# Performance work log

Measured on AMD Instinct MI355X. Metric: run time of the kernel, lower is better.

## Reference

```python
import jax, jax.numpy as jnp
import numpy as np

B, H, W, C = 4, 64, 64, 64
GROUPS = 32
EPS = 1e-3  # keras GroupNormalization default


def setup_inputs() -> dict:
    key = jax.random.key(0)
    ks = jax.random.split(key, 6)
    s = 1.0 / np.sqrt(C)
    return {
        'x': jax.random.normal(ks[0], (B, H, W, C), dtype=jnp.float32),
        'gamma': jnp.ones((C,), jnp.float32),
        'beta': jnp.zeros((C,), jnp.float32),
        'wq': jax.random.uniform(ks[1], (C, C), jnp.float32, -s, s),
        'bq': jnp.zeros((C,), jnp.float32),
        'wk': jax.random.uniform(ks[2], (C, C), jnp.float32, -s, s),
        'bk': jnp.zeros((C,), jnp.float32),
        'wv': jax.random.uniform(ks[3], (C, C), jnp.float32, -s, s),
        'bv': jnp.zeros((C,), jnp.float32),
        'wo': jnp.zeros((C, C), jnp.float32),  # init_scale=0.0 -> ~zero init
        'bo': jnp.zeros((C,), jnp.float32),
    }


def group_norm(x, gamma, beta):
    b, h, w, c = x.shape
    xg = x.reshape(b, h, w, GROUPS, c // GROUPS)
    mean = jnp.mean(xg, axis=(1, 2, 4), keepdims=True)
    var = jnp.var(xg, axis=(1, 2, 4), keepdims=True)
    xn = ((xg - mean) * jax.lax.rsqrt(var + EPS)).reshape(b, h, w, c)
    return xn * gamma + beta


def reference(x, gamma, beta, wq, bq, wk, bk, wv, bv, wo, bo):
    b, h, w, c = x.shape
    hn = group_norm(x, gamma, beta)
    # 1x1 convs == per-pixel dense layers
    q = jnp.einsum('bhwc,cd->bhwd', hn, wq) + bq
    k = jnp.einsum('bhwc,cd->bhwd', hn, wk) + bk
    v = jnp.einsum('bhwc,cd->bhwd', hn, wv) + bv
    # full spatial attention scores [B,H,W,H,W]
    scores = jnp.einsum('bhwc,bHWc->bhwHW', q, k) * (float(c) ** -0.5)
    attn = jax.nn.softmax(scores.reshape(b, h, w, h * w), axis=-1)
    attn = attn.reshape(b, h, w, h, w)
    o = jnp.einsum('bhwHW,bHWc->bhwc', attn, v)
    o = jnp.einsum('bhwc,cd->bhwd', o, wo) + bo
    return x + o
```

## Files before the change

kernel.cpp:

```cpp
#include <hip/hip_runtime.h>
#include <math.h>

#define BB 4
#define HH 64
#define WW 64
#define CC 64
#define NN (HH*WW)
#define NPIX (BB*NN)
#define EPS 1e-3f
#define QBLK 32
#define KSPLIT 8
#define NQT32 (NPIX/QBLK)
#define NCHK ((NN/KSPLIT)/64)

using bf16x8 = __attribute__((ext_vector_type(8))) short;
using f32x4  = __attribute__((ext_vector_type(4))) float;
using f32x16 = __attribute__((ext_vector_type(16))) float;

__device__ inline unsigned short bf16bits(float f) {
    union { float f; unsigned u; } a; a.f = f;
    unsigned r = a.u + 0x7fffu + ((a.u >> 16) & 1u);
    return (unsigned short)(r >> 16);
}
__device__ inline unsigned packbf(float lo, float hi) {
    return (unsigned)bf16bits(lo) | ((unsigned)bf16bits(hi) << 16);
}
__device__ inline unsigned cvtpk(float lo, float hi) {
    unsigned r;
    asm("v_cvt_pk_bf16_f32 %0, %1, %2" : "=v"(r) : "v"(lo), "v"(hi));
    return r;
}
#define PSWAP(a, b) asm("v_permlane32_swap_b32 %0, %1" : "+v"(a), "+v"(b))

__device__ __forceinline__ float exp2g(float x) { return exp2f(x); }

#define QSCALE 0.18033688011112042f

__global__ __launch_bounds__(256) void gn_wt(const float* __restrict__ x,
                                             float* __restrict__ part,
                                             const float* __restrict__ wq,
                                             const float* __restrict__ wk,
                                             const float* __restrict__ wv,
                                             const float* __restrict__ wo,
                                             short* __restrict__ wfrag) {
    int t = threadIdx.x;
    if (blockIdx.x < 256) {
        int c = t & 63, rr = t >> 6;
        int p0 = blockIdx.x * 64;
        float s = 0.f, s2 = 0.f;
        #pragma unroll
        for (int k = 0; k < 16; ++k) {
            float v = x[(size_t)(p0 + rr + 4 * k) * CC + c];
            s += v; s2 += v * v;
        }
        __shared__ float sA[256], sB[256];
        sA[t] = s; sB[t] = s2;
        __syncthreads();
        if (t < 64) {
            float fs  = sA[t] + sA[64 + t] + sA[128 + t] + sA[192 + t];
            float fs2 = sB[t] + sB[64 + t] + sB[128 + t] + sB[192 + t];
            part[blockIdx.x * 128 + t]      = fs;
            part[blockIdx.x * 128 + 64 + t] = fs2;
        }
    } else {
        const float* mats[3] = {wq, wk, wv};
        int i0 = (blockIdx.x - 256) * 256 + t;
        for (int e = i0; e < 12288; e += 16 * 256) {
            int m = e >> 12;
            int r = e & 4095;
            int dt = r >> 10, h = (r >> 9) & 1, lane = (r >> 3) & 63, j = r & 7;
            int g = lane >> 4, cl = lane & 15;
            float v = mats[m][(h * 32 + g * 8 + j) * 64 + dt * 16 + cl];
            wfrag[e] = (short)bf16bits(v);
        }
        for (int e = i0; e < 4096; e += 16 * 256) {
            int j = e & 7, lane = (e >> 3) & 63, dt = (e >> 9) & 1, s = e >> 10;
            int hi = lane >> 5, l31 = lane & 31;
            float v = wo[(8 * hi + 16 * s + j) * 64 + dt * 32 + l31];
            wfrag[12288 + e] = (short)bf16bits(v);
        }
    }
}

__global__ __launch_bounds__(256) void gn_final(const float* __restrict__ part,
                                                const float* __restrict__ gamma,
                                                const float* __restrict__ beta,
                                                float* __restrict__ scale,
                                                float* __restrict__ shift) {
    int b = blockIdx.x;
    int t = threadIdx.x;
    int c = t & 63, rr = t >> 6;
    float s = 0.f, s2 = 0.f;
    #pragma unroll
    for (int k = 0; k < 16; ++k) {
        int blk = b * 64 + rr + 4 * k;
        s  += part[blk * 128 + c];
        s2 += part[blk * 128 + 64 + c];
    }
    __shared__ float sA[256], sB[256];
    sA[t] = s; sB[t] = s2;
    __syncthreads();
    if (t < 64) {
        sA[t] = sA[t] + sA[64 + t] + sA[128 + t] + sA[192 + t];
        sB[t] = sB[t] + sB[64 + t] + sB[128 + t] + sB[192 + t];
    }
    __syncthreads();
    if (t < 64) {
        int g = t >> 1;
        float sumg  = sA[g * 2] + sA[g * 2 + 1];
        float sum2g = sB[g * 2] + sB[g * 2 + 1];
        const float n = (float)(NN * 2);
        float mean = sumg / n;
        float var  = sum2g / n - mean * mean;
        float r = rsqrtf(var + EPS);
        float a = gamma[t] * r;
        scale[b * CC + t] = a;
        shift[b * CC + t] = beta[t] - mean * a;
    }
}

__global__ __launch_bounds__(256) void qkv_proj(
        const float* __restrict__ x,
        const float* __restrict__ scale,
        const float* __restrict__ shift,
        const short* __restrict__ wfrag,
        const float* __restrict__ bq, const float* __restrict__ bk,
        const float* __restrict__ bv,
        short* __restrict__ qb, short* __restrict__ kb,
        short* __restrict__ vt) {
    __shared__ unsigned short vtile[64 * 72];
    int t = threadIdx.x;
    int lane = t & 63, wid = t >> 6;
    int g = lane >> 4, cl = lane & 15;
    int pixblk = blockIdx.x * 64;
    int pix0 = pixblk + wid * 16;
    int b = pixblk >> 12;

    const float* xp = x + (size_t)(pix0 + cl) * CC + g * 8;
    float4 x00 = *(const float4*)(xp);
    float4 x01 = *(const float4*)(xp + 4);
    float4 x10 = *(const float4*)(xp + 32);
    float4 x11 = *(const float4*)(xp + 36);
    const float* scb = scale + b * CC + g * 8;
    const float* sfb = shift + b * CC + g * 8;
    float4 s00 = *(const float4*)(scb);
    float4 s01 = *(const float4*)(scb + 4);
    float4 s10 = *(const float4*)(scb + 32);
    float4 s11 = *(const float4*)(scb + 36);
    float4 f00 = *(const float4*)(sfb);
    float4 f01 = *(const float4*)(sfb + 4);
    float4 f10 = *(const float4*)(sfb + 32);
    float4 f11 = *(const float4*)(sfb + 36);

    union { bf16x8 v; unsigned u[4]; } af0, af1;
    af0.u[0] = packbf(x00.x * s00.x + f00.x, x00.y * s00.y + f00.y);
    af0.u[1] = packbf(x00.z * s00.z + f00.z, x00.w * s00.w + f00.w);
    af0.u[2] = packbf(x01.x * s01.x + f01.x, x01.y * s01.y + f01.y);
    af0.u[3] = packbf(x01.z * s01.z + f01.z, x01.w * s01.w + f01.w);
    af1.u[0] = packbf(x10.x * s10.x + f10.x, x10.y * s10.y + f10.y);
    af1.u[1] = packbf(x10.z * s10.z + f10.z, x10.w * s10.w + f10.w);
    af1.u[2] = packbf(x11.x * s11.x + f11.x, x11.y * s11.y + f11.y);
    af1.u[3] = packbf(x11.z * s11.z + f11.z, x11.w * s11.w + f11.w);

    #pragma unroll
    for (int m = 0; m < 3; ++m) {
        const float* bias = (m == 0) ? bq : (m == 1) ? bk : bv;
        #pragma unroll
        for (int dt = 0; dt < 4; ++dt) {
            bf16x8 w0 = *(const bf16x8*)(wfrag + (size_t)(((m * 4 + dt) * 2 + 0) * 64 + lane) * 8);
            bf16x8 w1 = *(const bf16x8*)(wfrag + (size_t)(((m * 4 + dt) * 2 + 1) * 64 + lane) * 8);
            f32x4 z = (f32x4){0.f, 0.f, 0.f, 0.f};
            z = __builtin_amdgcn_mfma_f32_16x16x32_bf16(af0.v, w0, z, 0, 0, 0);
            z = __builtin_amdgcn_mfma_f32_16x16x32_bf16(af1.v, w1, z, 0, 0, 0);
            float bias_d = bias[dt * 16 + cl];
            if (m == 0) {
                #pragma unroll
                for (int r = 0; r < 4; ++r)
                    qb[(size_t)(pix0 + 4 * g + r) * CC + dt * 16 + cl] =
                        (short)bf16bits((z[r] + bias_d) * QSCALE);
            } else if (m == 1) {
                #pragma unroll
                for (int r = 0; r < 4; ++r)
                    kb[(size_t)(pix0 + 4 * g + r) * CC + dt * 16 + cl] =
                        (short)bf16bits(z[r] + bias_d);
            } else {
                #pragma unroll
                for (int r = 0; r < 4; ++r)
                    vtile[(dt * 16 + cl) * 72 + wid * 16 + 4 * g + r] =
                        bf16bits(z[r] + bias_d);
            }
        }
    }
    __syncthreads();
    {
        int d = t >> 2, seg = t & 3;
        uint4 v0 = *(const uint4*)(vtile + d * 72 + seg * 16);
        uint4 v1 = *(const uint4*)(vtile + d * 72 + seg * 16 + 8);
        uint4* dst = (uint4*)(vt + ((size_t)(b * 64 + d)) * NN + pixblk + seg * 16);
        dst[0] = v0; dst[1] = v1;
    }
}

__global__ __launch_bounds__(256, 4) void attn_mfma32(
        const short* __restrict__ qb, const short* __restrict__ kb,
        const short* __restrict__ vt,
        unsigned* __restrict__ obf, float* __restrict__ msb) {
    __shared__ short lds[2][2][64 * 64];
    const int t = threadIdx.x;
    const int lane = t & 63;
    const int wid  = t >> 6;
    const int hi  = lane >> 5;
    const int l31 = lane & 31;
    const int r7  = l31 & 7;
    const int kseg   = blockIdx.x & (KSPLIT - 1);
    const int qblock = blockIdx.x / KSPLIT;
    const int qtile  = qblock * 4 + wid;
    const int b = qtile >> 7;
    const int key0 = kseg * (NN / KSPLIT);

    bf16x8 qf[4];
    const short* qp = qb + (size_t)(qtile * QBLK + l31) * CC + 8 * hi;
    #pragma unroll
    for (int s = 0; s < 4; ++s) qf[s] = *(const bf16x8*)(qp + 16 * s);

    const int srow = t >> 3;
    const int scol = t & 7;
    const short* kS = kb + ((size_t)b * NN + key0) * CC;
    const short* vS = vt + ((size_t)b * CC) * NN + key0;

    f32x16 oacc0, oacc1;
    #pragma unroll
    for (int r = 0; r < 16; ++r) { oacc0[r] = 0.f; oacc1[r] = 0.f; }
    float psum = 0.f;

    auto stage = [&](int ck, int bsel) {
        #pragma unroll
        for (int r = 0; r < 2; ++r) {
            int row = srow + 32 * r;
            const short* src = kS + (size_t)(ck * 64 + row) * CC + (scol ^ (row & 7)) * 8;
            __builtin_amdgcn_global_load_lds(
                (const __attribute__((address_space(1))) void*)src,
                (__attribute__((address_space(3))) void*)&lds[bsel][0][(r * 32 + wid * 8) * 64],
                16, 0, 0);
        }
        #pragma unroll
        for (int r = 0; r < 2; ++r) {
            int row = srow + 32 * r;
            const short* src = vS + (size_t)row * NN + ck * 64 + (scol ^ (row & 7)) * 8;
            __builtin_amdgcn_global_load_lds(
                (const __attribute__((address_space(1))) void*)src,
                (__attribute__((address_space(3))) void*)&lds[bsel][1][(r * 32 + wid * 8) * 64],
                16, 0, 0);
        }
    };

    auto subbody = [&](const short* kB, const short* vB, int ks) {
        f32x16 st;
        #pragma unroll
        for (int r = 0; r < 16; ++r) st[r] = 0.f;
        __builtin_amdgcn_s_setprio(1);
        #pragma unroll
        for (int s = 0; s < 4; ++s) {
            bf16x8 kf = *(const bf16x8*)(kB + (32 * ks + l31) * 64 + ((2 * s + hi) ^ r7) * 8);
            st = __builtin_amdgcn_mfma_f32_32x32x16_bf16(kf, qf[s], st, 0, 0, 0);
        }
        __builtin_amdgcn_s_setprio(0);
        float p[16];
        float ps = 0.f;
        #pragma unroll
        for (int r = 0; r < 16; ++r) { p[r] = exp2g(st[r]); ps += p[r]; }
        psum += ps;
        unsigned w[8];
        #pragma unroll
        for (int i = 0; i < 8; ++i) w[i] = cvtpk(p[2 * i], p[2 * i + 1]);
        PSWAP(w[0], w[2]); PSWAP(w[1], w[3]);
        PSWAP(w[4], w[6]); PSWAP(w[5], w[7]);
        union { bf16x8 v; unsigned u[4]; } pa0, pa1;
        pa0.u[0] = w[0]; pa0.u[1] = w[1]; pa0.u[2] = w[2]; pa0.u[3] = w[3];
        pa1.u[0] = w[4]; pa1.u[1] = w[5]; pa1.u[2] = w[6]; pa1.u[3] = w[7];
        bf16x8 v00 = *(const bf16x8*)(vB + (l31) * 64      + ((4 * ks + 0 + hi) ^ r7) * 8);
        bf16x8 v10 = *(const bf16x8*)(vB + (32 + l31) * 64 + ((4 * ks + 0 + hi) ^ r7) * 8);
        bf16x8 v01 = *(const bf16x8*)(vB + (l31) * 64      + ((4 * ks + 2 + hi) ^ r7) * 8);
        bf16x8 v11 = *(const bf16x8*)(vB + (32 + l31) * 64 + ((4 * ks + 2 + hi) ^ r7) * 8);
        __builtin_amdgcn_s_setprio(1);
        oacc0 = __builtin_amdgcn_mfma_f32_32x32x16_bf16(pa0.v, v00, oacc0, 0, 0, 0);
        oacc1 = __builtin_amdgcn_mfma_f32_32x32x16_bf16(pa0.v, v10, oacc1, 0, 0, 0);
        oacc0 = __builtin_amdgcn_mfma_f32_32x32x16_bf16(pa1.v, v01, oacc0, 0, 0, 0);
        oacc1 = __builtin_amdgcn_mfma_f32_32x32x16_bf16(pa1.v, v11, oacc1, 0, 0, 0);
        __builtin_amdgcn_s_setprio(0);
    };

    stage(0, 0);
    #pragma unroll 2
    for (int c = 0; c < NCHK; ++c) {
        asm volatile("s_waitcnt vmcnt(0)" ::: "memory");
        __syncthreads();
        if (c + 1 < NCHK) stage(c + 1, (c + 1) & 1);
        const short* kB = &lds[c & 1][0][0];
        const short* vB = &lds[c & 1][1][0];
        subbody(kB, vB, 0);
        subbody(kB, vB, 1);
    }

    int task = qtile * KSPLIT + kseg;
    unsigned* ob32 = obf + (size_t)task * 1024;
    #pragma unroll
    for (int r = 0; r < 16; ++r) {
        int row = (r & 3) + 8 * (r >> 2) + 4 * hi;
        ob32[row * 32 + l31] = cvtpk(oacc0[r], oacc1[r]);
    }
    msb[task * 64 + lane] = psum;
}

__device__ __forceinline__ void acc2(float& lo_acc, float& hi_acc, unsigned u) {
    union { unsigned u; float f; } a, b;
    a.u = u << 16; b.u = u & 0xffff0000u;
    lo_acc += a.f; hi_acc += b.f;
}

__global__ __launch_bounds__(256) void attn_merge_outproj(
        const unsigned* __restrict__ obf, const float* __restrict__ msb,
        const short* __restrict__ wfrag,
        const float* __restrict__ x,
        const float* __restrict__ bo,
        float* __restrict__ out) {
    int t = threadIdx.x;
    int lane = t & 63, wid = t >> 6;
    int hi = lane >> 5, l31 = lane & 31;
    int qtile = blockIdx.x * 4 + wid;

    float stot = 0.f;
    #pragma unroll
    for (int s = 0; s < KSPLIT; ++s) {
        stot += msb[(qtile * KSPLIT + s) * 64 + l31]
              + msb[(qtile * KSPLIT + s) * 64 + 32 + l31];
    }
    float inv = 1.f / stot;

    float oa[4][8];
    #pragma unroll
    for (int s = 0; s < 4; ++s)
        #pragma unroll
        for (int j = 0; j < 8; ++j) oa[s][j] = 0.f;
    #pragma unroll 4
    for (int ks = 0; ks < KSPLIT; ++ks) {
        const unsigned* base = obf + (size_t)(qtile * KSPLIT + ks) * 1024 + l31 * 32 + 8 * hi;
        uint4 wa = *(const uint4*)(base);
        uint4 wb = *(const uint4*)(base + 4);
        uint4 wc = *(const uint4*)(base + 16);
        uint4 wd = *(const uint4*)(base + 20);
        acc2(oa[0][0], oa[2][0], wa.x); acc2(oa[0][1], oa[2][1], wa.y);
        acc2(oa[0][2], oa[2][2], wa.z); acc2(oa[0][3], oa[2][3], wa.w);
        acc2(oa[0][4], oa[2][4], wb.x); acc2(oa[0][5], oa[2][5], wb.y);
        acc2(oa[0][6], oa[2][6], wb.z); acc2(oa[0][7], oa[2][7], wb.w);
        acc2(oa[1][0], oa[3][0], wc.x); acc2(oa[1][1], oa[3][1], wc.y);
        acc2(oa[1][2], oa[3][2], wc.z); acc2(oa[1][3], oa[3][3], wc.w);
        acc2(oa[1][4], oa[3][4], wd.x); acc2(oa[1][5], oa[3][5], wd.y);
        acc2(oa[1][6], oa[3][6], wd.z); acc2(oa[1][7], oa[3][7], wd.w);
    }
    union { bf16x8 v; unsigned u[4]; } af[4];
    #pragma unroll
    for (int s = 0; s < 4; ++s)
        #pragma unroll
        for (int m = 0; m < 4; ++m)
            af[s].u[m] = cvtpk(oa[s][2 * m] * inv, oa[s][2 * m + 1] * inv);

    const short* w32 = wfrag + 12288;
    f32x16 z0, z1;
    #pragma unroll
    for (int r = 0; r < 16; ++r) { z0[r] = 0.f; z1[r] = 0.f; }
    #pragma unroll
    for (int s = 0; s < 4; ++s) {
        bf16x8 wb0 = *(const bf16x8*)(w32 + (size_t)((s * 2 + 0) * 64 + lane) * 8);
        bf16x8 wb1 = *(const bf16x8*)(w32 + (size_t)((s * 2 + 1) * 64 + lane) * 8);
        z0 = __builtin_amdgcn_mfma_f32_32x32x16_bf16(af[s].v, wb0, z0, 0, 0, 0);
        z1 = __builtin_amdgcn_mfma_f32_32x32x16_bf16(af[s].v, wb1, z1, 0, 0, 0);
    }
    float bo0 = bo[l31], bo1 = bo[32 + l31];
    #pragma unroll
    for (int r = 0; r < 16; ++r) {
        int row = (r & 3) + 8 * (r >> 2) + 4 * hi;
        size_t i0 = (size_t)(qtile * QBLK + row) * CC + l31;
        out[i0]      = x[i0]      + z0[r] + bo0;
        out[i0 + 32] = x[i0 + 32] + z1[r] + bo1;
    }
}

extern "C" void kernel_launch(void* const* d_in, const int* in_sizes, int n_in,
                              void* d_out, int out_size, void* d_ws, size_t ws_size,
                              hipStream_t stream) {
    const float* x     = (const float*)d_in[0];
    const float* gamma = (const float*)d_in[1];
    const float* beta  = (const float*)d_in[2];
    const float* wq    = (const float*)d_in[3];
    const float* bq    = (const float*)d_in[4];
    const float* wk    = (const float*)d_in[5];
    const float* bk    = (const float*)d_in[6];
    const float* wv    = (const float*)d_in[7];
    const float* bv    = (const float*)d_in[8];
    const float* wo    = (const float*)d_in[9];
    const float* bo    = (const float*)d_in[10];
    float* out = (float*)d_out;

    float* ws    = (float*)d_ws;
    float* scale = ws;
    float* shift = scale + 256;
    float* part  = shift + 256;
    short* wfrag = (short*)(part + 32768);
    short* qb    = wfrag + 16384;
    short* kbp   = qb  + (size_t)NPIX * CC;
    short* vtp   = kbp + (size_t)NPIX * CC;
    unsigned* obf = (unsigned*)(vtp + (size_t)NPIX * CC);
    float* msb   = (float*)(obf + (size_t)NQT32 * KSPLIT * 1024);

    hipLaunchKernelGGL(gn_wt, dim3(272), dim3(256), 0, stream,
                       x, part, wq, wk, wv, wo, wfrag);
    hipLaunchKernelGGL(gn_final, dim3(BB), dim3(256), 0, stream,
                       part, gamma, beta, scale, shift);
    hipLaunchKernelGGL(qkv_proj, dim3(256), dim3(256), 0, stream,
                       x, scale, shift, wfrag, bq, bk, bv, qb, kbp, vtp);
    hipLaunchKernelGGL(attn_mfma32, dim3(128 * KSPLIT), dim3(256), 0, stream,
                       qb, kbp, vtp, obf, msb);
    hipLaunchKernelGGL(attn_merge_outproj, dim3(NQT32 / 4), dim3(256), 0, stream,
                       obf, msb, wfrag, x, bo, out);
}
```

Before: 53.56 us.

## Process two query tiles per wave to reuse K/V fragments, raise key split

Each wave in the attention kernel now handles 64 queries (two 32-row Q tiles), so every K and V fragment read from LDS feeds twice as many MFMAs. This halves LDS traffic and staging per query. To keep enough blocks in flight, the key split rises to 16 when the workspace is large enough, otherwise it stays at 8. exp2 is replaced with a raw v_exp_f32 instruction. The cost is higher register pressure (launch bounds lowered to 3 blocks per SM) and a larger merge workload in the output-projection kernel.

```diff
diff --git a/kernel.cpp b/kernel.cpp
--- a/kernel.cpp
+++ b/kernel.cpp
@@ -9,9 +9,7 @@
 #define NPIX (BB*NN)
 #define EPS 1e-3f
 #define QBLK 32
-#define KSPLIT 8
 #define NQT32 (NPIX/QBLK)
-#define NCHK ((NN/KSPLIT)/64)
 
 using bf16x8 = __attribute__((ext_vector_type(8))) short;
 using f32x4  = __attribute__((ext_vector_type(4))) float;
@@ -32,7 +30,11 @@
 }
 #define PSWAP(a, b) asm("v_permlane32_swap_b32 %0, %1" : "+v"(a), "+v"(b))
 
-__device__ __forceinline__ float exp2g(float x) { return exp2f(x); }
+__device__ __forceinline__ float exp2g(float x) {
+    float r;
+    asm("v_exp_f32 %0, %1" : "=v"(r) : "v"(x));
+    return r;
+}
 
 #define QSCALE 0.18033688011112042f
 
@@ -201,7 +203,8 @@
     }
 }
 
-__global__ __launch_bounds__(256, 4) void attn_mfma32(
+template<int KS>
+__global__ __launch_bounds__(256, 3) void attn_mfma64(
         const short* __restrict__ qb, const short* __restrict__ kb,
         const short* __restrict__ vt,
         unsigned* __restrict__ obf, float* __restrict__ msb) {
@@ -212,26 +215,34 @@
     const int hi  = lane >> 5;
     const int l31 = lane & 31;
     const int r7  = l31 & 7;
-    const int kseg   = blockIdx.x & (KSPLIT - 1);
-    const int qblock = blockIdx.x / KSPLIT;
-    const int qtile  = qblock * 4 + wid;
-    const int b = qtile >> 7;
-    const int key0 = kseg * (NN / KSPLIT);
-
-    bf16x8 qf[4];
-    const short* qp = qb + (size_t)(qtile * QBLK + l31) * CC + 8 * hi;
-    #pragma unroll
-    for (int s = 0; s < 4; ++s) qf[s] = *(const bf16x8*)(qp + 16 * s);
+    const int kseg   = blockIdx.x % KS;
+    const int qblock = blockIdx.x / KS;
+    const int qt0 = (qblock * 4 + wid) * 2;
+    const int b = qblock >> 4;
+    const int key0 = kseg * (NN / KS);
+    const int NCHK = (NN / KS) / 64;
+
+    bf16x8 qf[2][4];
+    const short* qp = qb + (size_t)(qblock * 256 + wid * 64 + l31) * CC + 8 * hi;
+    #pragma unroll
+    for (int qc = 0; qc < 2; ++qc)
+        #pragma unroll
+        for (int s = 0; s < 4; ++s)
+            qf[qc][s] = *(const bf16x8*)(qp + qc * 32 * CC + 16 * s);
 
     const int srow = t >> 3;
     const int scol = t & 7;
     const short* kS = kb + ((size_t)b * NN + key0) * CC;
     const short* vS = vt + ((size_t)b * CC) * NN + key0;
 
-    f32x16 oacc0, oacc1;
-    #pragma unroll
-    for (int r = 0; r < 16; ++r) { oacc0[r] = 0.f; oacc1[r] = 0.f; }
-    float psum = 0.f;
+    f32x16 oacc[2][2];
+    #pragma unroll
+    for (int qc = 0; qc < 2; ++qc)
+        #pragma unroll
+        for (int dh = 0; dh < 2; ++dh)
+            #pragma unroll
+            for (int r = 0; r < 16; ++r) oacc[qc][dh][r] = 0.f;
+    float psum[2] = {0.f, 0.f};
 
     auto stage = [&](int ck, int bsel) {
         #pragma unroll
@@ -255,43 +266,47 @@
     };
 
     auto subbody = [&](const short* kB, const short* vB, int ks) {
-        f32x16 st;
-        #pragma unroll
-        for (int r = 0; r < 16; ++r) st[r] = 0.f;
-        __builtin_amdgcn_s_setprio(1);
-        #pragma unroll
-        for (int s = 0; s < 4; ++s) {
-            bf16x8 kf = *(const bf16x8*)(kB + (32 * ks + l31) * 64 + ((2 * s + hi) ^ r7) * 8);
-            st = __builtin_amdgcn_mfma_f32_32x32x16_bf16(kf, qf[s], st, 0, 0, 0);
-        }
-        __builtin_amdgcn_s_setprio(0);
-        float p[16];
-        float ps = 0.f;
-        #pragma unroll
-        for (int r = 0; r < 16; ++r) { p[r] = exp2g(st[r]); ps += p[r]; }
-        psum += ps;
-        unsigned w[8];
-        #pragma unroll
-        for (int i = 0; i < 8; ++i) w[i] = cvtpk(p[2 * i], p[2 * i + 1]);
-        PSWAP(w[0], w[2]); PSWAP(w[1], w[3]);
-        PSWAP(w[4], w[6]); PSWAP(w[5], w[7]);
-        union { bf16x8 v; unsigned u[4]; } pa0, pa1;
-        pa0.u[0] = w[0]; pa0.u[1] = w[1]; pa0.u[2] = w[2]; pa0.u[3] = w[3];
-        pa1.u[0] = w[4]; pa1.u[1] = w[5]; pa1.u[2] = w[6]; pa1.u[3] = w[7];
-        bf16x8 v00 = *(const bf16x8*)(vB + (l31) * 64      + ((4 * ks + 0 + hi) ^ r7) * 8);
-        bf16x8 v10 = *(const bf16x8*)(vB + (32 + l31) * 64 + ((4 * ks + 0 + hi) ^ r7) * 8);
-        bf16x8 v01 = *(const bf16x8*)(vB + (l31) * 64      + ((4 * ks + 2 + hi) ^ r7) * 8);
-        bf16x8 v11 = *(const bf16x8*)(vB + (32 + l31) * 64 + ((4 * ks + 2 + hi) ^ r7) * 8);
-        __builtin_amdgcn_s_setprio(1);
-        oacc0 = __builtin_amdgcn_mfma_f32_32x32x16_bf16(pa0.v, v00, oacc0, 0, 0, 0);
-        oacc1 = __builtin_amdgcn_mfma_f32_32x32x16_bf16(pa0.v, v10, oacc1, 0, 0, 0);
-        oacc0 = __builtin_amdgcn_mfma_f32_32x32x16_bf16(pa1.v, v01, oacc0, 0, 0, 0);
-        oacc1 = __builtin_amdgcn_mfma_f32_32x32x16_bf16(pa1.v, v11, oacc1, 0, 0, 0);
-        __builtin_amdgcn_s_setprio(0);
+        bf16x8 kf[4];
+        #pragma unroll
+        for (int s = 0; s < 4; ++s)
+            kf[s] = *(const bf16x8*)(kB + (32 * ks + l31) * 64 + ((2 * s + hi) ^ r7) * 8);
+        bf16x8 vf0 = *(const bf16x8*)(vB + (l31) * 64      + ((4 * ks + 0 + hi) ^ r7) * 8);
+        bf16x8 vf1 = *(const bf16x8*)(vB + (32 + l31) * 64 + ((4 * ks + 0 + hi) ^ r7) * 8);
+        bf16x8 vf2 = *(const bf16x8*)(vB + (l31) * 64      + ((4 * ks + 2 + hi) ^ r7) * 8);
+        bf16x8 vf3 = *(const bf16x8*)(vB + (32 + l31) * 64 + ((4 * ks + 2 + hi) ^ r7) * 8);
+        #pragma unroll
+        for (int qc = 0; qc < 2; ++qc) {
+            f32x16 st;
+            #pragma unroll
+            for (int r = 0; r < 16; ++r) st[r] = 0.f;
+            __builtin_amdgcn_s_setprio(1);
+            #pragma unroll
+            for (int s = 0; s < 4; ++s)
+                st = __builtin_amdgcn_mfma_f32_32x32x16_bf16(kf[s], qf[qc][s], st, 0, 0, 0);
+            __builtin_amdgcn_s_setprio(0);
+            float ps = 0.f;
+            #pragma unroll
+            for (int r = 0; r < 16; ++r) { st[r] = exp2g(st[r]); ps += st[r]; }
+            psum[qc] += ps;
+            unsigned w[8];
+            #pragma unroll
+            for (int i = 0; i < 8; ++i) w[i] = cvtpk(st[2 * i], st[2 * i + 1]);
+            PSWAP(w[0], w[2]); PSWAP(w[1], w[3]);
+            PSWAP(w[4], w[6]); PSWAP(w[5], w[7]);
+            union { bf16x8 v; unsigned u[4]; } pa0, pa1;
+            pa0.u[0] = w[0]; pa0.u[1] = w[1]; pa0.u[2] = w[2]; pa0.u[3] = w[3];
+            pa1.u[0] = w[4]; pa1.u[1] = w[5]; pa1.u[2] = w[6]; pa1.u[3] = w[7];
+            __builtin_amdgcn_s_setprio(1);
+            oacc[qc][0] = __builtin_amdgcn_mfma_f32_32x32x16_bf16(pa0.v, vf0, oacc[qc][0], 0, 0, 0);
+            oacc[qc][1] = __builtin_amdgcn_mfma_f32_32x32x16_bf16(pa0.v, vf1, oacc[qc][1], 0, 0, 0);
+            oacc[qc][0] = __builtin_amdgcn_mfma_f32_32x32x16_bf16(pa1.v, vf2, oacc[qc][0], 0, 0, 0);
+            oacc[qc][1] = __builtin_amdgcn_mfma_f32_32x32x16_bf16(pa1.v, vf3, oacc[qc][1], 0, 0, 0);
+            __builtin_amdgcn_s_setprio(0);
+        }
     };
 
     stage(0, 0);
-    #pragma unroll 2
+    #pragma unroll 1
     for (int c = 0; c < NCHK; ++c) {
         asm volatile("s_waitcnt vmcnt(0)" ::: "memory");
         __syncthreads();
@@ -302,14 +317,17 @@
         subbody(kB, vB, 1);
     }
 
-    int task = qtile * KSPLIT + kseg;
-    unsigned* ob32 = obf + (size_t)task * 1024;
-    #pragma unroll
-    for (int r = 0; r < 16; ++r) {
-        int row = (r & 3) + 8 * (r >> 2) + 4 * hi;
-        ob32[row * 32 + l31] = cvtpk(oacc0[r], oacc1[r]);
-    }
-    msb[task * 64 + lane] = psum;
+    #pragma unroll
+    for (int qc = 0; qc < 2; ++qc) {
+        int task = (qt0 + qc) * KS + kseg;
+        unsigned* ob32 = obf + (size_t)task * 1024;
+        #pragma unroll
+        for (int r = 0; r < 16; ++r) {
+            int row = (r & 3) + 8 * (r >> 2) + 4 * hi;
+            ob32[row * 32 + l31] = cvtpk(oacc[qc][0][r], oacc[qc][1][r]);
+        }
+        msb[task * 64 + lane] = psum[qc];
+    }
 }
 
 __device__ __forceinline__ void acc2(float& lo_acc, float& hi_acc, unsigned u) {
@@ -318,6 +336,7 @@
     lo_acc += a.f; hi_acc += b.f;
 }
 
+template<int KS>
 __global__ __launch_bounds__(256) void attn_merge_outproj(
         const unsigned* __restrict__ obf, const float* __restrict__ msb,
         const short* __restrict__ wfrag,
@@ -331,9 +350,9 @@
 
     float stot = 0.f;
     #pragma unroll
-    for (int s = 0; s < KSPLIT; ++s) {
-        stot += msb[(qtile * KSPLIT + s) * 64 + l31]
-              + msb[(qtile * KSPLIT + s) * 64 + 32 + l31];
+    for (int s = 0; s < KS; ++s) {
+        stot += msb[(qtile * KS + s) * 64 + l31]
+              + msb[(qtile * KS + s) * 64 + 32 + l31];
     }
     float inv = 1.f / stot;
 
@@ -343,8 +362,8 @@
         #pragma unroll
         for (int j = 0; j < 8; ++j) oa[s][j] = 0.f;
     #pragma unroll 4
-    for (int ks = 0; ks < KSPLIT; ++ks) {
-        const unsigned* base = obf + (size_t)(qtile * KSPLIT + ks) * 1024 + l31 * 32 + 8 * hi;
+    for (int ks = 0; ks < KS; ++ks) {
+        const unsigned* base = obf + (size_t)(qtile * KS + ks) * 1024 + l31 * 32 + 8 * hi;
         uint4 wa = *(const uint4*)(base);
         uint4 wb = *(const uint4*)(base + 4);
         uint4 wc = *(const uint4*)(base + 16);
@@ -411,7 +430,11 @@
     short* kbp   = qb  + (size_t)NPIX * CC;
     short* vtp   = kbp + (size_t)NPIX * CC;
     unsigned* obf = (unsigned*)(vtp + (size_t)NPIX * CC);
-    float* msb   = (float*)(obf + (size_t)NQT32 * KSPLIT * 1024);
+
+    const size_t fixed_bytes = 2048 + 131072 + 32768 + 3 * (size_t)NPIX * CC * 2;
+    const size_t need16 = fixed_bytes + (size_t)NQT32 * 16 * 1024 * 4
+                        + (size_t)NQT32 * 16 * 64 * 4;
+    const bool use16 = (ws_size >= need16);
 
     hipLaunchKernelGGL(gn_wt, dim3(272), dim3(256), 0, stream,
                        x, part, wq, wk, wv, wo, wfrag);
@@ -419,8 +442,17 @@
                        part, gamma, beta, scale, shift);
     hipLaunchKernelGGL(qkv_proj, dim3(256), dim3(256), 0, stream,
                        x, scale, shift, wfrag, bq, bk, bv, qb, kbp, vtp);
-    hipLaunchKernelGGL(attn_mfma32, dim3(128 * KSPLIT), dim3(256), 0, stream,
-                       qb, kbp, vtp, obf, msb);
-    hipLaunchKernelGGL(attn_merge_outproj, dim3(NQT32 / 4), dim3(256), 0, stream,
-                       obf, msb, wfrag, x, bo, out);
-}
+    if (use16) {
+        float* msb = (float*)(obf + (size_t)NQT32 * 16 * 1024);
+        hipLaunchKernelGGL((attn_mfma64<16>), dim3(64 * 16), dim3(256), 0, stream,
+                           qb, kbp, vtp, obf, msb);
+        hipLaunchKernelGGL((attn_merge_outproj<16>), dim3(NQT32 / 4), dim3(256), 0, stream,
+                           obf, msb, wfrag, x, bo, out);
+    } else {
+        float* msb = (float*)(obf + (size_t)NQT32 * 8 * 1024);
+        hipLaunchKernelGGL((attn_mfma64<8>), dim3(64 * 8), dim3(256), 0, stream,
+                           qb, kbp, vtp, obf, msb);
+        hipLaunchKernelGGL((attn_merge_outproj<8>), dim3(NQT32 / 4), dim3(256), 0, stream,
+                           obf, msb, wfrag, x, bo, out);
+    }
+}
```

New measurement: 85.80 us. 60.2% more time.
